# Kernel optimization log

Measured on AMD Instinct MI355X. Metric: run time of the kernel, lower is better.

## Reference

```python
import jax, jax.numpy as jnp
import numpy as np

# Dimensions (see FeatureMixer.__init__ / forward)
B, Q, H, P, C_HEAD = 4, 900, 4, 32, 64          # C_HEAD = feats_dim // num_heads
FEATS_DIM, QUERY_DIM, E = 256, 256, 2
EP = E * P                                        # 64 expanded points
PARAM1 = FEATS_DIM * EP                           # 16384
PARAM2 = EP * P * H                               # 8192
TOTAL = PARAM1 + PARAM2                           # 24576
D1 = PARAM1 // (H * C_HEAD)                       # 64 hidden dim after channel mixing
OUT_IN = PARAM2 * E                               # 16384 = H*EP*D1, out_proj in_features
EPS = 1e-5


def _ln2d(x):
    # F.layer_norm over the last two dims, no affine
    m = jnp.mean(x, axis=(-2, -1), keepdims=True)
    v = jnp.mean((x - m) ** 2, axis=(-2, -1), keepdims=True)
    return (x - m) * jax.lax.rsqrt(v + EPS)


def setup_inputs() -> dict:
    key = jax.random.key(0)
    ks = jax.random.split(key, 6)
    return {
        "query_feats": jax.random.normal(ks[0], (B, Q, QUERY_DIM), jnp.float32),
        "sampled_features": jax.random.normal(ks[1], (B, Q, H, P, C_HEAD), jnp.float32),
        "W_gen": jax.random.normal(ks[2], (QUERY_DIM, TOTAL), jnp.float32) * 0.02,
        "b_gen": jax.random.normal(ks[3], (TOTAL,), jnp.float32) * 0.02,
        "W_out": jax.random.normal(ks[4], (OUT_IN, QUERY_DIM), jnp.float32) * 0.02,
        "b_out": jnp.zeros((QUERY_DIM,), jnp.float32),
        "ln_w": jnp.ones((QUERY_DIM,), jnp.float32),
        "ln_b": jnp.zeros((QUERY_DIM,), jnp.float32),
    }


def reference(query_feats, sampled_features, W_gen, b_gen, W_out, b_out, ln_w, ln_b):
    # generate per-query mixing parameters: (B,Q,TOTAL)
    params = query_feats @ W_gen + b_gen
    p1 = params[..., :PARAM1].reshape(B, Q, H, C_HEAD, D1)   # channel mixer
    p2 = params[..., PARAM1:].reshape(B, Q, H, EP, P)        # spatial mixer

    # channel mixing: (B,Q,H,P,C) @ (B,Q,H,C,D1) -> (B,Q,H,P,D1)
    out = jnp.einsum('bqhpc,bqhcd->bqhpd', sampled_features, p1)
    out = _ln2d(jax.nn.gelu(out, approximate=False))

    # spatial mixing: (B,Q,H,EP,P) @ (B,Q,H,P,D1) -> (B,Q,H,EP,D1)
    out = jnp.einsum('bqhep,bqhpd->bqhed', p2, out)
    out = _ln2d(jax.nn.gelu(out, approximate=False))

    # project back to query dim + affine LayerNorm
    out = out.reshape(B, Q, OUT_IN) @ W_out + b_out
    m = jnp.mean(out, axis=-1, keepdims=True)
    v = jnp.mean((out - m) ** 2, axis=-1, keepdims=True)
    return (out - m) * jax.lax.rsqrt(v + EPS) * ln_w + ln_b
```

## Files before the change

kernel.cpp:

```cpp
#include <hip/hip_runtime.h>
#include <hip/hip_bf16.h>


typedef __attribute__((ext_vector_type(8))) __bf16 bf16x8;
typedef __attribute__((ext_vector_type(4))) float f32x4;
typedef __attribute__((ext_vector_type(4))) short short4v;
typedef __attribute__((ext_vector_type(8))) short short8v;

#define BQ_TOT 3600

__device__ __forceinline__ short f2bf(float f) {
  __hip_bfloat16 h = __float2bfloat16(f);
  short s; __builtin_memcpy(&s, &h, 2);
  return s;
}
__device__ __forceinline__ bf16x8 pack8(float4 a, float4 b) {
  short8v o;
  o[0] = f2bf(a.x); o[1] = f2bf(a.y); o[2] = f2bf(a.z); o[3] = f2bf(a.w);
  o[4] = f2bf(b.x); o[5] = f2bf(b.y); o[6] = f2bf(b.z); o[7] = f2bf(b.w);
  return __builtin_bit_cast(bf16x8, o);
}
__device__ __forceinline__ float gelu_f(float x) {
  float x2 = x * x;
  float u = x * (0.7978845608f + 0.0356774081f * x2);
  float e = __builtin_amdgcn_exp2f(u * 2.885390082f);
  float t = 1.0f - 2.0f / (e + 1.0f);
  return 0.5f * x * (1.0f + t);
}
__device__ __forceinline__ void wred2(float& a, float& b) {
#pragma unroll
  for (int m = 32; m >= 1; m >>= 1) {
    a += __shfl_xor(a, m, 64);
    b += __shfl_xor(b, m, 64);
  }
}

__global__ __launch_bounds__(256) void ktrans_f2b(const float* __restrict__ in,
                                                  short* __restrict__ out,
                                                  int R, int C) {
  __shared__ float t[32][33];
  int tx = threadIdx.x & 31, ty = threadIdx.x >> 5;
  int r0 = blockIdx.y * 32, c0 = blockIdx.x * 32;
#pragma unroll
  for (int i = 0; i < 4; i++)
    t[ty + i * 8][tx] = in[(size_t)(r0 + ty + i * 8) * C + c0 + tx];
  __syncthreads();
#pragma unroll
  for (int i = 0; i < 4; i++)
    out[(size_t)(c0 + ty + i * 8) * R + r0 + tx] = f2bf(t[tx][ty + i * 8]);
}

__global__ __launch_bounds__(256) void k1t_gemm(const float* __restrict__ X,
                                                const short* __restrict__ WT,
                                                const float* __restrict__ bg,
                                                short* __restrict__ par,
                                                int nrows) {
  __shared__ short smem[128 * 40 * 2];
  short* As = smem;
  short* Bs = smem + 128 * 40;
  const int tid = threadIdx.x;
  const int rt = blockIdx.x, ct = blockIdx.y;
  const int lane = tid & 63, wv = tid >> 6;
  const int l15 = lane & 15, quad = lane >> 4;
  const int wm = (wv & 1) * 64, wn = (wv >> 1) * 64;
  const int sm = tid >> 1, sk = (tid & 1) * 16;
  f32x4 acc[4][4] = {};
  for (int k0 = 0; k0 < 256; k0 += 32) {
    float4 av[4] = {};
    int gr = rt * 128 + sm;
    if (gr < nrows) {
      const float4* pa = (const float4*)(X + (size_t)gr * 256 + k0 + sk);
      av[0] = pa[0]; av[1] = pa[1]; av[2] = pa[2]; av[3] = pa[3];
    }
    *(short8v*)(void*)(As + sm * 40 + sk) = __builtin_bit_cast(short8v, pack8(av[0], av[1]));
    *(short8v*)(void*)(As + sm * 40 + sk + 8) = __builtin_bit_cast(short8v, pack8(av[2], av[3]));
    const uint4* pb = (const uint4*)(WT + (size_t)(ct * 128 + sm) * 256 + k0 + sk);
    *(uint4*)(Bs + sm * 40 + sk) = pb[0];
    *(uint4*)(Bs + sm * 40 + sk + 8) = pb[1];
    __syncthreads();
    bf16x8 af[4], bfr[4];
#pragma unroll
    for (int i = 0; i < 4; i++)
      af[i] = *(const bf16x8*)(const void*)(As + (wm + i * 16 + l15) * 40 + quad * 8);
#pragma unroll
    for (int j = 0; j < 4; j++)
      bfr[j] = *(const bf16x8*)(const void*)(Bs + (wn + j * 16 + l15) * 40 + quad * 8);
#pragma unroll
    for (int i = 0; i < 4; i++)
#pragma unroll
      for (int j = 0; j < 4; j++)
        acc[i][j] = __builtin_amdgcn_mfma_f32_16x16x32_bf16(af[i], bfr[j], acc[i][j], 0, 0, 0);
    __syncthreads();
  }
  short* Cs = smem;
#pragma unroll
  for (int h = 0; h < 2; h++) {
    if ((wv & 1) == h) {
#pragma unroll
      for (int i = 0; i < 4; i++)
#pragma unroll
        for (int j = 0; j < 4; j++) {
          float bgv = bg[ct * 128 + wn + j * 16 + l15];
#pragma unroll
          for (int r = 0; r < 4; r++)
            Cs[(i * 16 + quad * 4 + r) * 136 + wn + j * 16 + l15] =
                f2bf(acc[i][j][r] + bgv);
        }
    }
    __syncthreads();
#pragma unroll
    for (int it = 0; it < 4; it++) {
      int rr = it * 16 + (tid >> 4);
      int cc = (tid & 15) * 8;
      uint4 v = *(const uint4*)(const void*)(Cs + rr * 136 + cc);
      int row = rt * 128 + h * 64 + rr;
      if (row < nrows)
        *(uint4*)(par + (size_t)row * 24576 + ct * 128 + cc) = v;
    }
    __syncthreads();
  }
}

__global__ __launch_bounds__(256) void k1_gemm(const float* __restrict__ X,
                                               const float* __restrict__ Wg,
                                               const float* __restrict__ bg,
                                               short* __restrict__ par,
                                               int nrows) {
  __shared__ short As[128 * 40];
  __shared__ short Bs[128 * 40];
  const int tid = threadIdx.x;
  const int rt = blockIdx.x, ct = blockIdx.y;
  const int lane = tid & 63, wv = tid >> 6;
  const int l15 = lane & 15, quad = lane >> 4;
  const int wm = (wv & 1) * 64, wn = (wv >> 1) * 64;
  const int sm = tid >> 1, sk = (tid & 1) * 16;
  const int bk = tid >> 3, bn0 = (tid & 7) * 16;
  f32x4 acc[4][4] = {};
  for (int k0 = 0; k0 < 256; k0 += 32) {
    float4 av[4] = {};
    int gr = rt * 128 + sm;
    if (gr < nrows) {
      const float4* pa = (const float4*)(X + (size_t)gr * 256 + k0 + sk);
      av[0] = pa[0]; av[1] = pa[1]; av[2] = pa[2]; av[3] = pa[3];
    }
    *(short8v*)(void*)(As + sm * 40 + sk) = __builtin_bit_cast(short8v, pack8(av[0], av[1]));
    *(short8v*)(void*)(As + sm * 40 + sk + 8) = __builtin_bit_cast(short8v, pack8(av[2], av[3]));
    const float4* pb = (const float4*)(Wg + (size_t)(k0 + bk) * 24576 + ct * 128 + bn0);
    float4 b0 = pb[0], b1 = pb[1], b2 = pb[2], b3 = pb[3];
    short* bd = Bs + bn0 * 40 + bk;
    bd[0 * 40] = f2bf(b0.x); bd[1 * 40] = f2bf(b0.y); bd[2 * 40] = f2bf(b0.z); bd[3 * 40] = f2bf(b0.w);
    bd[4 * 40] = f2bf(b1.x); bd[5 * 40] = f2bf(b1.y); bd[6 * 40] = f2bf(b1.z); bd[7 * 40] = f2bf(b1.w);
    bd[8 * 40] = f2bf(b2.x); bd[9 * 40] = f2bf(b2.y); bd[10 * 40] = f2bf(b2.z); bd[11 * 40] = f2bf(b2.w);
    bd[12 * 40] = f2bf(b3.x); bd[13 * 40] = f2bf(b3.y); bd[14 * 40] = f2bf(b3.z); bd[15 * 40] = f2bf(b3.w);
    __syncthreads();
    bf16x8 af[4], bfr[4];
#pragma unroll
    for (int i = 0; i < 4; i++)
      af[i] = *(const bf16x8*)(const void*)(As + (wm + i * 16 + l15) * 40 + quad * 8);
#pragma unroll
    for (int j = 0; j < 4; j++)
      bfr[j] = *(const bf16x8*)(const void*)(Bs + (wn + j * 16 + l15) * 40 + quad * 8);
#pragma unroll
    for (int i = 0; i < 4; i++)
#pragma unroll
      for (int j = 0; j < 4; j++)
        acc[i][j] = __builtin_amdgcn_mfma_f32_16x16x32_bf16(af[i], bfr[j], acc[i][j], 0, 0, 0);
    __syncthreads();
  }
#pragma unroll
  for (int i = 0; i < 4; i++) {
#pragma unroll
    for (int j = 0; j < 4; j++) {
      int col = ct * 128 + wn + j * 16 + l15;
      float bgv = bg[col];
#pragma unroll
      for (int r = 0; r < 4; r++) {
        int row = rt * 128 + wm + i * 16 + quad * 4 + r;
        if (row < nrows)
          par[(size_t)row * 24576 + col] = f2bf(acc[i][j][r] + bgv);
      }
    }
  }
}

__global__ __launch_bounds__(64, 3) void k2_mixw(const float* __restrict__ sf,
                                                 const short* __restrict__ par,
                                                 short* __restrict__ U) {
  __shared__ short p1T[64 * 68];
  __shared__ short Tl[64 * 40];
  const int bq = blockIdx.x >> 2, hd = blockIdx.x & 3;
  const int lane = threadIdx.x & 63;
  const int l15 = lane & 15, quad = lane >> 4;
  const short* pp1 = par + (size_t)bq * 24576 + hd * 4096;
#pragma unroll
  for (int it = 0; it < 8; it++) {
    int c = it * 8 + (lane >> 3);
    int d0 = (lane & 7) * 8;
    short8v tv = *(const short8v*)(const void*)(pp1 + c * 64 + d0);
#pragma unroll
    for (int i = 0; i < 8; i++) p1T[(d0 + i) * 68 + c] = tv[i];
  }
  __syncthreads();
  const float* psf = sf + (size_t)bq * 8192 + hd * 2048;
  bf16x8 sa[2][2];
#pragma unroll
  for (int tm = 0; tm < 2; tm++)
#pragma unroll
    for (int kk = 0; kk < 2; kk++) {
      const float* p = psf + (tm * 16 + l15) * 64 + kk * 32 + quad * 8;
      sa[tm][kk] = pack8(*(const float4*)p, *(const float4*)(p + 4));
    }
  f32x4 acc1[2][4] = {};
#pragma unroll
  for (int kk = 0; kk < 2; kk++) {
#pragma unroll
    for (int tn = 0; tn < 4; tn++) {
      const short* bp = p1T + (tn * 16 + l15) * 68 + kk * 32 + quad * 8;
      short4v lo = *(const short4v*)(const void*)bp;
      short4v hi = *(const short4v*)(const void*)(bp + 4);
      bf16x8 bfr = __builtin_bit_cast(bf16x8, __builtin_shufflevector(lo, hi, 0, 1, 2, 3, 4, 5, 6, 7));
#pragma unroll
      for (int tm = 0; tm < 2; tm++)
        acc1[tm][tn] = __builtin_amdgcn_mfma_f32_16x16x32_bf16(sa[tm][kk], bfr, acc1[tm][tn], 0, 0, 0);
    }
  }
  float s1 = 0.f, s2 = 0.f;
#pragma unroll
  for (int tm = 0; tm < 2; tm++)
#pragma unroll
    for (int tn = 0; tn < 4; tn++)
#pragma unroll
      for (int r = 0; r < 4; r++) {
        float g = gelu_f(acc1[tm][tn][r]);
        acc1[tm][tn][r] = g;
        s1 += g; s2 += g * g;
      }
  wred2(s1, s2);
  float mean = s1 * (1.f / 2048.f);
  float rstd = rsqrtf(fmaxf(s2 * (1.f / 2048.f) - mean * mean, 0.f) + 1e-5f);
#pragma unroll
  for (int tm = 0; tm < 2; tm++)
#pragma unroll
    for (int tn = 0; tn < 4; tn++) {
      short4v o;
#pragma unroll
      for (int r = 0; r < 4; r++) o[r] = f2bf((acc1[tm][tn][r] - mean) * rstd);
      *(short4v*)(void*)(Tl + (tn * 16 + l15) * 40 + tm * 16 + quad * 4) = o;
    }
  __syncthreads();
  const short* pp2 = par + (size_t)bq * 24576 + 16384 + hd * 2048;
  bf16x8 a2[4], b2[4];
#pragma unroll
  for (int t = 0; t < 4; t++) {
    a2[t] = *(const bf16x8*)(const void*)(pp2 + (t * 16 + l15) * 32 + quad * 8);
    b2[t] = *(const bf16x8*)(const void*)(Tl + (t * 16 + l15) * 40 + quad * 8);
  }
  f32x4 acc2[4][4] = {};
#pragma unroll
  for (int tm = 0; tm < 4; tm++)
#pragma unroll
    for (int tn = 0; tn < 4; tn++)
      acc2[tm][tn] = __builtin_amdgcn_mfma_f32_16x16x32_bf16(a2[tm], b2[tn], acc2[tm][tn], 0, 0, 0);
  float u1 = 0.f, u2 = 0.f;
#pragma unroll
  for (int tm = 0; tm < 4; tm++)
#pragma unroll
    for (int tn = 0; tn < 4; tn++)
#pragma unroll
      for (int r = 0; r < 4; r++) {
        float g = gelu_f(acc2[tm][tn][r]);
        acc2[tm][tn][r] = g;
        u1 += g; u2 += g * g;
      }
  wred2(u1, u2);
  float m2 = u1 * (1.f / 4096.f);
  float rs2 = rsqrtf(fmaxf(u2 * (1.f / 4096.f) - m2 * m2, 0.f) + 1e-5f);
  short* pu = U + (size_t)bq * 16384 + hd * 4096;
#pragma unroll
  for (int h2 = 0; h2 < 2; h2++) {
    __syncthreads();
#pragma unroll
    for (int tmh = 0; tmh < 2; tmh++) {
      int tm = h2 * 2 + tmh;
#pragma unroll
      for (int tn = 0; tn < 4; tn++)
#pragma unroll
        for (int r = 0; r < 4; r++) {
          int er = tmh * 16 + quad * 4 + r;
          Tl[er * 72 + tn * 16 + l15] = f2bf((acc2[tm][tn][r] - m2) * rs2);
        }
    }
    __syncthreads();
#pragma unroll
    for (int i = 0; i < 4; i++) {
      int er = i * 8 + (lane >> 3);
      int dch = (lane & 7) * 8;
      uint4 v = *(const uint4*)(const void*)(Tl + er * 72 + dch);
      *(uint4*)(void*)(pu + (size_t)(h2 * 32 + er) * 64 + dch) = v;
    }
  }
}

__global__ __launch_bounds__(256) void k3t_gemm(const short* __restrict__ U,
                                                const short* __restrict__ WT,
                                                float* __restrict__ C2p,
                                                int nrows) {
  __shared__ short As[64 * 72];
  __shared__ short Bs[64 * 72];
  const int tid = threadIdx.x;
  const int bm = blockIdx.x, bn = blockIdx.y, seg = blockIdx.z;
  const int lane = tid & 63, wv = tid >> 6;
  const int l15 = lane & 15, quad = lane >> 4;
  const int wm = (wv & 1) * 32, wn = (wv >> 1) * 32;
  const int sr = tid >> 2, sk = (tid & 3) * 16;
  f32x4 acc[2][2] = {};
  int k0 = seg * 4096;
  for (int kt = 0; kt < 64; kt++, k0 += 64) {
    uint4 a0 = {0, 0, 0, 0}, a1 = {0, 0, 0, 0};
    int gr = bm * 64 + sr;
    if (gr < nrows) {
      const uint4* pa = (const uint4*)(U + (size_t)gr * 16384 + k0 + sk);
      a0 = pa[0]; a1 = pa[1];
    }
    *(uint4*)(As + sr * 72 + sk) = a0;
    *(uint4*)(As + sr * 72 + sk + 8) = a1;
    const uint4* pb = (const uint4*)(WT + (size_t)(bn * 64 + sr) * 16384 + k0 + sk);
    *(uint4*)(Bs + sr * 72 + sk) = pb[0];
    *(uint4*)(Bs + sr * 72 + sk + 8) = pb[1];
    __syncthreads();
#pragma unroll
    for (int kk = 0; kk < 64; kk += 32) {
      bf16x8 af[2], bfr[2];
#pragma unroll
      for (int i = 0; i < 2; i++)
        af[i] = *(const bf16x8*)(const void*)(As + (wm + i * 16 + l15) * 72 + kk + quad * 8);
#pragma unroll
      for (int j = 0; j < 2; j++)
        bfr[j] = *(const bf16x8*)(const void*)(Bs + (wn + j * 16 + l15) * 72 + kk + quad * 8);
#pragma unroll
      for (int i = 0; i < 2; i++)
#pragma unroll
        for (int j = 0; j < 2; j++)
          acc[i][j] = __builtin_amdgcn_mfma_f32_16x16x32_bf16(af[i], bfr[j], acc[i][j], 0, 0, 0);
    }
    __syncthreads();
  }
#pragma unroll
  for (int i = 0; i < 2; i++)
#pragma unroll
    for (int j = 0; j < 2; j++)
#pragma unroll
      for (int r = 0; r < 4; r++) {
        int row = bm * 64 + wm + i * 16 + quad * 4 + r;
        if (row < nrows)
          C2p[((size_t)seg * nrows + row) * 256 + bn * 64 + wn + j * 16 + l15] = acc[i][j][r];
      }
}

__global__ __launch_bounds__(256) void k3_gemm(const short* __restrict__ U,
                                               const float* __restrict__ Wo,
                                               float* __restrict__ C2p,
                                               int nrows) {
  __shared__ short As[64 * 72];
  __shared__ short Bs[64 * 72];
  const int tid = threadIdx.x;
  const int bm = blockIdx.x, bn = blockIdx.y, seg = blockIdx.z;
  const int lane = tid & 63, wv = tid >> 6;
  const int l15 = lane & 15, quad = lane >> 4;
  const int wm = (wv & 1) * 32, wn = (wv >> 1) * 32;
  const int sr = tid >> 2, sk = (tid & 3) * 16;
  const int bk = tid >> 2, bn0 = (tid & 3) * 16;
  f32x4 acc[2][2] = {};
  int k0 = seg * 4096;
  for (int kt = 0; kt < 64; kt++, k0 += 64) {
    uint4 a0 = {0, 0, 0, 0}, a1 = {0, 0, 0, 0};
    int gr = bm * 64 + sr;
    if (gr < nrows) {
      const uint4* pa = (const uint4*)(U + (size_t)gr * 16384 + k0 + sk);
      a0 = pa[0]; a1 = pa[1];
    }
    *(uint4*)(As + sr * 72 + sk) = a0;
    *(uint4*)(As + sr * 72 + sk + 8) = a1;
    const float4* pb = (const float4*)(Wo + (size_t)(k0 + bk) * 256 + bn * 64 + bn0);
    float4 b0 = pb[0], b1 = pb[1], b2 = pb[2], b3 = pb[3];
    short* bd = Bs + bn0 * 72 + bk;
    bd[0 * 72] = f2bf(b0.x); bd[1 * 72] = f2bf(b0.y); bd[2 * 72] = f2bf(b0.z); bd[3 * 72] = f2bf(b0.w);
    bd[4 * 72] = f2bf(b1.x); bd[5 * 72] = f2bf(b1.y); bd[6 * 72] = f2bf(b1.z); bd[7 * 72] = f2bf(b1.w);
    bd[8 * 72] = f2bf(b2.x); bd[9 * 72] = f2bf(b2.y); bd[10 * 72] = f2bf(b2.z); bd[11 * 72] = f2bf(b2.w);
    bd[12 * 72] = f2bf(b3.x); bd[13 * 72] = f2bf(b3.y); bd[14 * 72] = f2bf(b3.z); bd[15 * 72] = f2bf(b3.w);
    __syncthreads();
#pragma unroll
    for (int kk = 0; kk < 64; kk += 32) {
      bf16x8 af[2], bfr[2];
#pragma unroll
      for (int i = 0; i < 2; i++)
        af[i] = *(const bf16x8*)(const void*)(As + (wm + i * 16 + l15) * 72 + kk + quad * 8);
#pragma unroll
      for (int j = 0; j < 2; j++)
        bfr[j] = *(const bf16x8*)(const void*)(Bs + (wn + j * 16 + l15) * 72 + kk + quad * 8);
#pragma unroll
      for (int i = 0; i < 2; i++)
#pragma unroll
        for (int j = 0; j < 2; j++)
          acc[i][j] = __builtin_amdgcn_mfma_f32_16x16x32_bf16(af[i], bfr[j], acc[i][j], 0, 0, 0);
    }
    __syncthreads();
  }
#pragma unroll
  for (int i = 0; i < 2; i++)
#pragma unroll
    for (int j = 0; j < 2; j++)
#pragma unroll
      for (int r = 0; r < 4; r++) {
        int row = bm * 64 + wm + i * 16 + quad * 4 + r;
        if (row < nrows)
          C2p[((size_t)seg * nrows + row) * 256 + bn * 64 + wn + j * 16 + l15] = acc[i][j][r];
      }
}

__global__ __launch_bounds__(256) void k4_ln(const float* __restrict__ C2p,
                                             const float* __restrict__ bo,
                                             const float* __restrict__ lnw,
                                             const float* __restrict__ lnb,
                                             float* __restrict__ out,
                                             int nrows) {
  int row = blockIdx.x * 4 + (threadIdx.x >> 6);
  if (row >= nrows) return;
  int lane = threadIdx.x & 63;
  float v[4] = {0.f, 0.f, 0.f, 0.f};
#pragma unroll
  for (int s = 0; s < 4; s++) {
    const float4* p = (const float4*)(C2p + ((size_t)s * nrows + row) * 256) + lane;
    float4 t = *p;
    v[0] += t.x; v[1] += t.y; v[2] += t.z; v[3] += t.w;
  }
  float4 bov = *((const float4*)bo + lane);
  v[0] += bov.x; v[1] += bov.y; v[2] += bov.z; v[3] += bov.w;
  float s1 = v[0] + v[1] + v[2] + v[3];
  float s2 = v[0] * v[0] + v[1] * v[1] + v[2] * v[2] + v[3] * v[3];
  wred2(s1, s2);
  float mean = s1 * (1.f / 256.f);
  float rstd = rsqrtf(fmaxf(s2 * (1.f / 256.f) - mean * mean, 0.f) + 1e-5f);
  float4 wv = *((const float4*)lnw + lane);
  float4 bv = *((const float4*)lnb + lane);
  float4 o;
  o.x = (v[0] - mean) * rstd * wv.x + bv.x;
  o.y = (v[1] - mean) * rstd * wv.y + bv.y;
  o.z = (v[2] - mean) * rstd * wv.z + bv.z;
  o.w = (v[3] - mean) * rstd * wv.w + bv.w;
  *((float4*)(out + (size_t)row * 256) + lane) = o;
}

extern "C" void kernel_launch(void* const* d_in, const int* in_sizes, int n_in,
                              void* d_out, int out_size, void* d_ws, size_t ws_size,
                              hipStream_t stream) {
  const float* qf  = (const float*)d_in[0];
  const float* sf  = (const float*)d_in[1];
  const float* Wg  = (const float*)d_in[2];
  const float* bg  = (const float*)d_in[3];
  const float* Wo  = (const float*)d_in[4];
  const float* bo  = (const float*)d_in[5];
  const float* lnw = (const float*)d_in[6];
  const float* lnb = (const float*)d_in[7];
  char* wsb = (char*)d_ws;

  const size_t sz_par = (size_t)BQ_TOT * 24576 * 2;
  const size_t sz_U   = (size_t)BQ_TOT * 16384 * 2;
  const size_t sz_C2  = (size_t)4 * BQ_TOT * 256 * 4;
  const size_t sz_WTg = (size_t)24576 * 256 * 2;
  const size_t sz_WTo = (size_t)16384 * 256 * 2;
  const size_t NEED   = sz_WTg + sz_WTo + sz_par + sz_U + sz_C2;

  if (ws_size >= NEED) {
    short* WTg = (short*)wsb;
    short* WTo = (short*)(wsb + sz_WTg);
    short* par = (short*)(wsb + sz_WTg + sz_WTo);
    short* Uc  = (short*)(wsb + sz_WTg + sz_WTo + sz_par);
    float* C2p = (float*)(wsb + sz_WTg + sz_WTo + sz_par + sz_U);
    ktrans_f2b<<<dim3(768, 8), 256, 0, stream>>>(Wg, WTg, 256, 24576);
    ktrans_f2b<<<dim3(8, 512), 256, 0, stream>>>(Wo, WTo, 16384, 256);
    k1t_gemm<<<dim3(29, 192), 256, 0, stream>>>(qf, WTg, bg, par, BQ_TOT);
    k2_mixw<<<dim3(BQ_TOT * 4), 64, 0, stream>>>(sf, par, Uc);
    k3t_gemm<<<dim3(57, 4, 4), 256, 0, stream>>>(Uc, WTo, C2p, BQ_TOT);
    k4_ln<<<dim3(900), 256, 0, stream>>>(C2p, bo, lnw, lnb, (float*)d_out, BQ_TOT);
  } else {
    const size_t per_row = 86016;
    long long chunk_ll = (long long)(ws_size / per_row);
    int chunk = (chunk_ll > BQ_TOT) ? BQ_TOT : (int)chunk_ll;
    if (chunk < 8) chunk = 8;
    short* par = (short*)wsb;
    short* Uc  = (short*)(wsb + (size_t)chunk * 24576 * 2);
    float* C2p = (float*)(wsb + (size_t)chunk * 24576 * 2 + (size_t)chunk * 16384 * 2);
    for (int rb = 0; rb < BQ_TOT; rb += chunk) {
      int r = (BQ_TOT - rb < chunk) ? (BQ_TOT - rb) : chunk;
      k1_gemm<<<dim3((r + 127) / 128, 192), 256, 0, stream>>>(
          qf + (size_t)rb * 256, Wg, bg, par, r);
      k2_mixw<<<dim3(r * 4), 64, 0, stream>>>(sf + (size_t)rb * 8192, par, Uc);
      k3_gemm<<<dim3((r + 63) / 64, 4, 4), 256, 0, stream>>>(Uc, Wo, C2p, r);
      k4_ln<<<dim3((r + 3) / 4), 256, 0, stream>>>(
          C2p, bo, lnw, lnb, (float*)d_out + (size_t)rb * 256, r);
    }
  }
}
```

Baseline: 511.1 us.

## Pre-convert query to bf16, remap GEMM blocks per XCD, widen out-proj tiles with 16-way split-K

Adds a pre-pass that converts query_feats to bf16 once, so the parameter-generating GEMM loads bf16 tiles directly instead of converting floats in every column tile. Its launch becomes a flat grid remapped so that each XCD handles a contiguous range of weight column tiles, which should improve L2 reuse of WT. The output-projection GEMM now computes all 256 output columns per block with 16 K-segments instead of 4, so the activation tile U is read once rather than four times. The partial sums go into the dead par buffer to save workspace, at the cost of a 16-way reduction in the LayerNorm kernel.

```diff
diff --git a/kernel.cpp b/kernel.cpp
--- a/kernel.cpp
+++ b/kernel.cpp
@@ -35,6 +35,13 @@
   }
 }
 
+__global__ __launch_bounds__(256) void kcvt_f2b(const float* __restrict__ in,
+                                                short* __restrict__ out) {
+  int idx = (blockIdx.x * 256 + threadIdx.x) * 8;
+  const float4* p = (const float4*)(in + idx);
+  *(short8v*)(void*)(out + idx) = __builtin_bit_cast(short8v, pack8(p[0], p[1]));
+}
+
 __global__ __launch_bounds__(256) void ktrans_f2b(const float* __restrict__ in,
                                                   short* __restrict__ out,
                                                   int R, int C) {
@@ -50,7 +57,7 @@
     out[(size_t)(c0 + ty + i * 8) * R + r0 + tx] = f2bf(t[tx][ty + i * 8]);
 }
 
-__global__ __launch_bounds__(256) void k1t_gemm(const float* __restrict__ X,
+__global__ __launch_bounds__(256) void k1t_gemm(const short* __restrict__ Xb,
                                                 const short* __restrict__ WT,
                                                 const float* __restrict__ bg,
                                                 short* __restrict__ par,
@@ -58,38 +65,41 @@
   __shared__ short smem[128 * 40 * 2];
   short* As = smem;
   short* Bs = smem + 128 * 40;
+  const int b = blockIdx.x;
+  const int xcd = b & 7, i = b >> 3;
+  const int ct = xcd * 24 + i / 29;
+  const int rt = i % 29;
   const int tid = threadIdx.x;
-  const int rt = blockIdx.x, ct = blockIdx.y;
   const int lane = tid & 63, wv = tid >> 6;
   const int l15 = lane & 15, quad = lane >> 4;
   const int wm = (wv & 1) * 64, wn = (wv >> 1) * 64;
   const int sm = tid >> 1, sk = (tid & 1) * 16;
   f32x4 acc[4][4] = {};
   for (int k0 = 0; k0 < 256; k0 += 32) {
-    float4 av[4] = {};
+    uint4 a0 = {0, 0, 0, 0}, a1 = {0, 0, 0, 0};
     int gr = rt * 128 + sm;
     if (gr < nrows) {
-      const float4* pa = (const float4*)(X + (size_t)gr * 256 + k0 + sk);
-      av[0] = pa[0]; av[1] = pa[1]; av[2] = pa[2]; av[3] = pa[3];
-    }
-    *(short8v*)(void*)(As + sm * 40 + sk) = __builtin_bit_cast(short8v, pack8(av[0], av[1]));
-    *(short8v*)(void*)(As + sm * 40 + sk + 8) = __builtin_bit_cast(short8v, pack8(av[2], av[3]));
+      const uint4* pa = (const uint4*)(Xb + (size_t)gr * 256 + k0 + sk);
+      a0 = pa[0]; a1 = pa[1];
+    }
+    *(uint4*)(As + sm * 40 + sk) = a0;
+    *(uint4*)(As + sm * 40 + sk + 8) = a1;
     const uint4* pb = (const uint4*)(WT + (size_t)(ct * 128 + sm) * 256 + k0 + sk);
     *(uint4*)(Bs + sm * 40 + sk) = pb[0];
     *(uint4*)(Bs + sm * 40 + sk + 8) = pb[1];
     __syncthreads();
     bf16x8 af[4], bfr[4];
 #pragma unroll
-    for (int i = 0; i < 4; i++)
-      af[i] = *(const bf16x8*)(const void*)(As + (wm + i * 16 + l15) * 40 + quad * 8);
+    for (int i2 = 0; i2 < 4; i2++)
+      af[i2] = *(const bf16x8*)(const void*)(As + (wm + i2 * 16 + l15) * 40 + quad * 8);
 #pragma unroll
     for (int j = 0; j < 4; j++)
       bfr[j] = *(const bf16x8*)(const void*)(Bs + (wn + j * 16 + l15) * 40 + quad * 8);
 #pragma unroll
-    for (int i = 0; i < 4; i++)
+    for (int i2 = 0; i2 < 4; i2++)
 #pragma unroll
       for (int j = 0; j < 4; j++)
-        acc[i][j] = __builtin_amdgcn_mfma_f32_16x16x32_bf16(af[i], bfr[j], acc[i][j], 0, 0, 0);
+        acc[i2][j] = __builtin_amdgcn_mfma_f32_16x16x32_bf16(af[i2], bfr[j], acc[i2][j], 0, 0, 0);
     __syncthreads();
   }
   short* Cs = smem;
@@ -97,14 +107,14 @@
   for (int h = 0; h < 2; h++) {
     if ((wv & 1) == h) {
 #pragma unroll
-      for (int i = 0; i < 4; i++)
+      for (int i2 = 0; i2 < 4; i2++)
 #pragma unroll
         for (int j = 0; j < 4; j++) {
           float bgv = bg[ct * 128 + wn + j * 16 + l15];
 #pragma unroll
           for (int r = 0; r < 4; r++)
-            Cs[(i * 16 + quad * 4 + r) * 136 + wn + j * 16 + l15] =
-                f2bf(acc[i][j][r] + bgv);
+            Cs[(i2 * 16 + quad * 4 + r) * 136 + wn + j * 16 + l15] =
+                f2bf(acc[i2][j][r] + bgv);
         }
     }
     __syncthreads();
@@ -301,21 +311,22 @@
   }
 }
 
-__global__ __launch_bounds__(256) void k3t_gemm(const short* __restrict__ U,
+__global__ __launch_bounds__(256) void k3x_gemm(const short* __restrict__ U,
                                                 const short* __restrict__ WT,
                                                 float* __restrict__ C2p,
                                                 int nrows) {
   __shared__ short As[64 * 72];
-  __shared__ short Bs[64 * 72];
+  __shared__ short Bs[256 * 72];
+  const int b = blockIdx.x;
+  const int seg = b & 15, bm = b >> 4;
   const int tid = threadIdx.x;
-  const int bm = blockIdx.x, bn = blockIdx.y, seg = blockIdx.z;
   const int lane = tid & 63, wv = tid >> 6;
   const int l15 = lane & 15, quad = lane >> 4;
-  const int wm = (wv & 1) * 32, wn = (wv >> 1) * 32;
+  const int wn = wv * 64;
   const int sr = tid >> 2, sk = (tid & 3) * 16;
-  f32x4 acc[2][2] = {};
-  int k0 = seg * 4096;
-  for (int kt = 0; kt < 64; kt++, k0 += 64) {
+  f32x4 acc[4][4] = {};
+  int k0 = seg * 1024;
+  for (int kt = 0; kt < 16; kt++, k0 += 64) {
     uint4 a0 = {0, 0, 0, 0}, a1 = {0, 0, 0, 0};
     int gr = bm * 64 + sr;
     if (gr < nrows) {
@@ -324,36 +335,40 @@
     }
     *(uint4*)(As + sr * 72 + sk) = a0;
     *(uint4*)(As + sr * 72 + sk + 8) = a1;
-    const uint4* pb = (const uint4*)(WT + (size_t)(bn * 64 + sr) * 16384 + k0 + sk);
-    *(uint4*)(Bs + sr * 72 + sk) = pb[0];
-    *(uint4*)(Bs + sr * 72 + sk + 8) = pb[1];
+#pragma unroll
+    for (int rr = 0; rr < 4; rr++) {
+      int br = rr * 64 + sr;
+      const uint4* pb = (const uint4*)(WT + (size_t)br * 16384 + k0 + sk);
+      *(uint4*)(Bs + br * 72 + sk) = pb[0];
+      *(uint4*)(Bs + br * 72 + sk + 8) = pb[1];
+    }
     __syncthreads();
 #pragma unroll
     for (int kk = 0; kk < 64; kk += 32) {
-      bf16x8 af[2], bfr[2];
-#pragma unroll
-      for (int i = 0; i < 2; i++)
-        af[i] = *(const bf16x8*)(const void*)(As + (wm + i * 16 + l15) * 72 + kk + quad * 8);
-#pragma unroll
-      for (int j = 0; j < 2; j++)
+      bf16x8 af[4], bfr[4];
+#pragma unroll
+      for (int i = 0; i < 4; i++)
+        af[i] = *(const bf16x8*)(const void*)(As + (i * 16 + l15) * 72 + kk + quad * 8);
+#pragma unroll
+      for (int j = 0; j < 4; j++)
         bfr[j] = *(const bf16x8*)(const void*)(Bs + (wn + j * 16 + l15) * 72 + kk + quad * 8);
 #pragma unroll
-      for (int i = 0; i < 2; i++)
-#pragma unroll
-        for (int j = 0; j < 2; j++)
+      for (int i = 0; i < 4; i++)
+#pragma unroll
+        for (int j = 0; j < 4; j++)
           acc[i][j] = __builtin_amdgcn_mfma_f32_16x16x32_bf16(af[i], bfr[j], acc[i][j], 0, 0, 0);
     }
     __syncthreads();
   }
 #pragma unroll
-  for (int i = 0; i < 2; i++)
-#pragma unroll
-    for (int j = 0; j < 2; j++)
+  for (int i = 0; i < 4; i++)
+#pragma unroll
+    for (int j = 0; j < 4; j++)
 #pragma unroll
       for (int r = 0; r < 4; r++) {
-        int row = bm * 64 + wm + i * 16 + quad * 4 + r;
+        int row = bm * 64 + i * 16 + quad * 4 + r;
         if (row < nrows)
-          C2p[((size_t)seg * nrows + row) * 256 + bn * 64 + wn + j * 16 + l15] = acc[i][j][r];
+          C2p[((size_t)seg * nrows + row) * 256 + wn + j * 16 + l15] = acc[i][j][r];
       }
 }
 
@@ -423,13 +438,12 @@
                                              const float* __restrict__ lnw,
                                              const float* __restrict__ lnb,
                                              float* __restrict__ out,
-                                             int nrows) {
+                                             int nrows, int nseg) {
   int row = blockIdx.x * 4 + (threadIdx.x >> 6);
   if (row >= nrows) return;
   int lane = threadIdx.x & 63;
   float v[4] = {0.f, 0.f, 0.f, 0.f};
-#pragma unroll
-  for (int s = 0; s < 4; s++) {
+  for (int s = 0; s < nseg; s++) {
     const float4* p = (const float4*)(C2p + ((size_t)s * nrows + row) * 256) + lane;
     float4 t = *p;
     v[0] += t.x; v[1] += t.y; v[2] += t.z; v[3] += t.w;
@@ -464,25 +478,27 @@
   const float* lnb = (const float*)d_in[7];
   char* wsb = (char*)d_ws;
 
+  const size_t sz_WTg = (size_t)24576 * 256 * 2;
+  const size_t sz_WTo = (size_t)16384 * 256 * 2;
   const size_t sz_par = (size_t)BQ_TOT * 24576 * 2;
   const size_t sz_U   = (size_t)BQ_TOT * 16384 * 2;
-  const size_t sz_C2  = (size_t)4 * BQ_TOT * 256 * 4;
-  const size_t sz_WTg = (size_t)24576 * 256 * 2;
-  const size_t sz_WTo = (size_t)16384 * 256 * 2;
-  const size_t NEED   = sz_WTg + sz_WTo + sz_par + sz_U + sz_C2;
+  const size_t sz_Xb  = (size_t)BQ_TOT * 256 * 2;
+  const size_t NEED   = sz_WTg + sz_WTo + sz_par + sz_U + sz_Xb;
 
   if (ws_size >= NEED) {
     short* WTg = (short*)wsb;
     short* WTo = (short*)(wsb + sz_WTg);
     short* par = (short*)(wsb + sz_WTg + sz_WTo);
     short* Uc  = (short*)(wsb + sz_WTg + sz_WTo + sz_par);
-    float* C2p = (float*)(wsb + sz_WTg + sz_WTo + sz_par + sz_U);
+    short* Xb  = (short*)(wsb + sz_WTg + sz_WTo + sz_par + sz_U);
+    float* C2p = (float*)par;
     ktrans_f2b<<<dim3(768, 8), 256, 0, stream>>>(Wg, WTg, 256, 24576);
     ktrans_f2b<<<dim3(8, 512), 256, 0, stream>>>(Wo, WTo, 16384, 256);
-    k1t_gemm<<<dim3(29, 192), 256, 0, stream>>>(qf, WTg, bg, par, BQ_TOT);
+    kcvt_f2b<<<dim3(450), 256, 0, stream>>>(qf, Xb);
+    k1t_gemm<<<dim3(5568), 256, 0, stream>>>(Xb, WTg, bg, par, BQ_TOT);
     k2_mixw<<<dim3(BQ_TOT * 4), 64, 0, stream>>>(sf, par, Uc);
-    k3t_gemm<<<dim3(57, 4, 4), 256, 0, stream>>>(Uc, WTo, C2p, BQ_TOT);
-    k4_ln<<<dim3(900), 256, 0, stream>>>(C2p, bo, lnw, lnb, (float*)d_out, BQ_TOT);
+    k3x_gemm<<<dim3(912), 256, 0, stream>>>(Uc, WTo, C2p, BQ_TOT);
+    k4_ln<<<dim3(900), 256, 0, stream>>>(C2p, bo, lnw, lnb, (float*)d_out, BQ_TOT, 16);
   } else {
     const size_t per_row = 86016;
     long long chunk_ll = (long long)(ws_size / per_row);
@@ -498,7 +514,7 @@
       k2_mixw<<<dim3(r * 4), 64, 0, stream>>>(sf + (size_t)rb * 8192, par, Uc);
       k3_gemm<<<dim3((r + 63) / 64, 4, 4), 256, 0, stream>>>(Uc, Wo, C2p, r);
       k4_ln<<<dim3((r + 3) / 4), 256, 0, stream>>>(
-          C2p, bo, lnw, lnb, (float*)d_out + (size_t)rb * 256, r);
-    }
-  }
-}
+          C2p, bo, lnw, lnb, (float*)d_out + (size_t)rb * 256, r, 4);
+    }
+  }
+}
```

Measured after the change: 455.5 us. 1.12x faster.
